# Kernel tuning notes

Hardware: AMD Instinct MI355X
Metric: run time of the kernel (lower is better)

## Reference

```python
import jax, jax.numpy as jnp
import numpy as np
import math

N = 10000      # nodes (batched protein residues)
E = 160000     # edges (avg degree 16)
D = 1280       # node/hidden dim (ESM2-650M)
M = 24         # message_dim
EE = 16        # edge_embedding_dim (sinusoidal distance features)
L = 6          # num EGNN layers
LN_EPS = 1e-5


def setup_inputs() -> dict:
    key = jax.random.key(0)
    ks = jax.random.split(key, 20)
    s = 0.02
    h = jax.random.normal(ks[0], (N, D), jnp.float32)
    pos = jax.random.normal(ks[1], (N, 3), jnp.float32) * 10.0
    edge_index = jax.random.randint(ks[2], (2, E), 0, N, jnp.int32)
    msg_in_dim = 2 * D + EE + 1  # h_i, h_j, edge_attr, radial
    params = dict(
        node_emb_W=jax.random.normal(ks[3], (D, D), jnp.float32) * s,
        node_emb_b=jnp.zeros((D,), jnp.float32),
        msg_W1=jax.random.normal(ks[4], (L, msg_in_dim, M), jnp.float32) * s,
        msg_b1=jnp.zeros((L, M), jnp.float32),
        msg_W2=jax.random.normal(ks[5], (L, M, M), jnp.float32) * s,
        msg_b2=jnp.zeros((L, M), jnp.float32),
        coord_W1=jax.random.normal(ks[6], (L - 1, M, M), jnp.float32) * s,
        coord_b1=jnp.zeros((L - 1, M), jnp.float32),
        coord_W2=jax.random.normal(ks[7], (L - 1, M, 1), jnp.float32) * s,  # no bias
        node_W1=jax.random.normal(ks[8], (L, D + M, M), jnp.float32) * s,
        node_b1=jnp.zeros((L, M), jnp.float32),
        node_W2=jax.random.normal(ks[9], (L, M, D), jnp.float32) * s,
        node_b2=jnp.zeros((L, D), jnp.float32),
        ln_g=jnp.ones((L, D), jnp.float32),
        ln_b=jnp.zeros((L, D), jnp.float32),
    )
    return dict(h=h, pos=pos, edge_index=edge_index, **params)


def reference(h, pos, edge_index, node_emb_W, node_emb_b, msg_W1, msg_b1,
              msg_W2, msg_b2, coord_W1, coord_b1, coord_W2,
              node_W1, node_b1, node_W2, node_b2, ln_g, ln_b):
    row, col = edge_index[0], edge_index[1]  # PyG: row=source j, col=target i

    # sinusoidal distance embedding from initial coordinates (computed once)
    freqs = jnp.exp(-math.log(10000.0) * jnp.arange(0, EE, 2, dtype=jnp.float32) / EE)
    d0 = pos[row] - pos[col]                      # (E,3)
    dist = jnp.sqrt(jnp.sum(d0 * d0, axis=1))     # (E,)
    ang = dist[:, None] * freqs[None, :]          # (E, EE/2)
    edge_attr = jnp.stack([jnp.sin(ang), jnp.cos(ang)], axis=2).reshape(dist.shape[0], EE)

    h = h @ node_emb_W + node_emb_b

    # mean-aggregation denominator: in-degree of target nodes, clamped to 1
    deg = jax.ops.segment_sum(jnp.ones_like(dist), col, num_segments=N)
    denom = jnp.maximum(deg, 1.0)[:, None]

    for l in range(L):
        cd = pos[row] - pos[col]                  # (E,3) coord_diff
        radial = jnp.sum(cd * cd, axis=1, keepdims=True)
        msg_in = jnp.concatenate([h[col], h[row], edge_attr, radial], axis=-1)  # (E, 2D+EE+1)
        msg = jax.nn.silu(jax.nn.silu(msg_in @ msg_W1[l] + msg_b1[l]) @ msg_W2[l] + msg_b2[l])
        msg_agg = jax.ops.segment_sum(msg, col, num_segments=N) / denom  # scatter-mean
        if l < L - 1:  # update_coords for all but last layer
            w = jax.nn.silu(msg @ coord_W1[l] + coord_b1[l]) @ coord_W2[l]  # (E,1)
            pos = pos + jax.ops.segment_sum(cd * w, col, num_segments=N)   # index_add
        h_up = jax.nn.silu(jnp.concatenate([h, msg_agg], axis=-1) @ node_W1[l] + node_b1[l]) @ node_W2[l] + node_b2[l]
        hn = h + h_up
        mu = jnp.mean(hn, axis=-1, keepdims=True)
        var = jnp.mean((hn - mu) ** 2, axis=-1, keepdims=True)
        h = (hn - mu) / jnp.sqrt(var + LN_EPS) * ln_g[l] + ln_b[l]
        # dropout is identity in eval mode
    return h, pos
```

## Files before the change

### kernel.cpp

```cpp
#include <hip/hip_runtime.h>

#define NN 10000
#define NE 160000
#define DD 1280
#define MM 24

typedef __attribute__((ext_vector_type(8))) short bf16x8;
typedef __attribute__((ext_vector_type(4))) float f32x4;
typedef unsigned short u16;

#define O_nembW 0
#define O_nembB 1638400
#define O_msgW1 1639680
#define O_msgB1 2010880
#define O_msgW2 2011136
#define O_msgB2 2014592
#define O_cW1   2014848
#define O_cB1   2017792
#define O_cW2   2017920
#define O_nW1   2018048
#define O_nB1   2205824
#define O_nW2   2206080
#define O_nB2   2390400
#define O_lnG   2398080
#define O_lnB   2405760
#define TOTW    2413440

__device__ __forceinline__ float b2f(u16 u){
  union { unsigned int i; float f; } v; v.i = ((unsigned int)u) << 16; return v.f;
}
__device__ __forceinline__ u16 f2b(float f){
  union { float f; unsigned int i; } v; v.f = f;
  return (u16)((v.i + 0x7fffu + ((v.i >> 16) & 1u)) >> 16);
}
__device__ __forceinline__ float silu_f(float x){ return x / (1.f + __expf(-x)); }

__device__ __forceinline__ void gll16(const u16* g, u16* l){
  __builtin_amdgcn_global_load_lds(
      (const __attribute__((address_space(1))) void*)g,
      (__attribute__((address_space(3))) void*)l, 16, 0, 0);
}

__global__ __launch_bounds__(256) void k_sniff(const u16* __restrict__ h0, int* __restrict__ modep)
{
  __shared__ int cnt;
  if (threadIdx.x == 0) cnt = 0;
  __syncthreads();
  int local = 0;
  for (int i = threadIdx.x; i < 16384; i += 256){
    unsigned int e = (h0[i] >> 7) & 0xFF;
    if (e >= 0xE0) local++;
  }
  atomicAdd(&cnt, local);
  __syncthreads();
  if (threadIdx.x == 0) *modep = (cnt > 16) ? 0 : 1;
}

__global__ __launch_bounds__(256) void k_cvtw(const int* __restrict__ modep,
    const void* p0, const void* p1, const void* p2, const void* p3, const void* p4,
    const void* p5, const void* p6, const void* p7, const void* p8, const void* p9,
    const void* p10, const void* p11, const void* p12, const void* p13, const void* p14,
    u16* __restrict__ wbf)
{
  int i = blockIdx.x * 256 + threadIdx.x;
  if (i >= TOTW) return;
  int mode = *modep;
  const void* src; int j; int sz;
  if      (i < O_nembB){ src = p0;  j = i - O_nembW; sz = 1638400; }
  else if (i < O_msgW1){ src = p1;  j = i - O_nembB; sz = 1280; }
  else if (i < O_msgB1){ src = p2;  j = i - O_msgW1; sz = 371088; }
  else if (i < O_msgW2){ src = p3;  j = i - O_msgB1; sz = 144; }
  else if (i < O_msgB2){ src = p4;  j = i - O_msgW2; sz = 3456; }
  else if (i < O_cW1)  { src = p5;  j = i - O_msgB2; sz = 144; }
  else if (i < O_cB1)  { src = p6;  j = i - O_cW1;   sz = 2880; }
  else if (i < O_cW2)  { src = p7;  j = i - O_cB1;   sz = 120; }
  else if (i < O_nW1)  { src = p8;  j = i - O_cW2;   sz = 120; }
  else if (i < O_nB1)  { src = p9;  j = i - O_nW1;   sz = 187776; }
  else if (i < O_nW2)  { src = p10; j = i - O_nB1;   sz = 144; }
  else if (i < O_nB2)  { src = p11; j = i - O_nW2;   sz = 184320; }
  else if (i < O_lnG)  { src = p12; j = i - O_nB2;   sz = 7680; }
  else if (i < O_lnB)  { src = p13; j = i - O_lnG;   sz = 7680; }
  else                 { src = p14; j = i - O_lnB;   sz = 7680; }
  u16 v = 0;
  if (j < sz) v = mode ? ((const u16*)src)[j] : f2b(((const float*)src)[j]);
  wbf[i] = v;
}

__global__ __launch_bounds__(256) void k_tr(const u16* __restrict__ win, u16* __restrict__ wout)
{
  __shared__ u16 tile[32][33];
  int bx = blockIdx.x % 40, by = blockIdx.x / 40;
  int tc = threadIdx.x & 31, tr = threadIdx.x >> 5;
  #pragma unroll
  for (int p = 0; p < 4; p++){
    int r = p*8 + tr;
    tile[r][tc] = win[(size_t)(by*32 + r)*1280 + bx*32 + tc];
  }
  __syncthreads();
  #pragma unroll
  for (int p = 0; p < 4; p++){
    int r = p*8 + tr;
    wout[(size_t)(bx*32 + r)*1280 + by*32 + tc] = tile[tc][r];
  }
}

__global__ __launch_bounds__(256) void k_packproj(const u16* __restrict__ wbf, u16* __restrict__ wproj)
{
  int i = blockIdx.x * 256 + threadIdx.x;
  if (i >= 6*80*1280) return;
  int l = i / (80*1280);
  int rem = i - l*80*1280;
  int n = rem / 1280;
  int k = rem - n*1280;
  u16 v = 0;
  if (n < 24)       v = wbf[O_msgW1 + (size_t)l*2577*24 + (size_t)k*24 + n];
  else if (n < 48)  v = wbf[O_msgW1 + (size_t)l*2577*24 + (size_t)(1280+k)*24 + (n-24)];
  else if (n < 72)  v = wbf[O_nW1   + (size_t)l*1304*24 + (size_t)k*24 + (n-48)];
  wproj[i] = v;
}

__global__ __launch_bounds__(256) void k_packw2(const u16* __restrict__ wbf, u16* __restrict__ wn2p)
{
  int i = blockIdx.x * 256 + threadIdx.x;
  int l = i / (1280*32); int rem = i - l*1280*32;
  int n = rem >> 5, k = rem & 31;
  wn2p[i] = (k < 24) ? wbf[O_nW2 + (size_t)l*24*1280 + (size_t)k*1280 + n] : (u16)0;
}

__global__ __launch_bounds__(256) void k_cvth(const void* h0, const int* __restrict__ modep,
                                              u16* __restrict__ h0b)
{
  int i = blockIdx.x * 256 + threadIdx.x;
  if (*modep){
    ((int4*)h0b)[i] = ((const int4*)h0)[i];
  } else {
    const float* s = (const float*)h0 + (size_t)i*8;
    bf16x8 o;
    #pragma unroll
    for (int j = 0; j < 8; j++) o[j] = (short)f2b(s[j]);
    *(bf16x8*)(h0b + (size_t)i*8) = o;
  }
}

__global__ __launch_bounds__(256) void k_setup(const void* pos0, const int* __restrict__ modep,
    float* __restrict__ deg, float* __restrict__ posf, float* __restrict__ posf0)
{
  int i = blockIdx.x * 256 + threadIdx.x;
  int mode = *modep;
  if (i < NN) deg[i] = 0.f;
  if (i < NN * 3){
    float p = mode ? b2f(((const u16*)pos0)[i]) : ((const float*)pos0)[i];
    posf[i] = p; posf0[i] = p;
  }
}

__global__ __launch_bounds__(256) void k_deg(const int* __restrict__ eidx, float* __restrict__ deg)
{
  int e = blockIdx.x * 256 + threadIdx.x;
  atomicAdd(&deg[eidx[NE + e]], 1.f);
}

__global__ __launch_bounds__(256) void k_prefix(const float* __restrict__ deg,
                                                int* __restrict__ offs, int* __restrict__ cursor)
{
  __shared__ int part[256];
  int t = threadIdx.x;
  int lo = t * 40, hi = lo + 40; if (hi > NN) hi = NN; if (lo > NN) lo = NN;
  int s = 0;
  for (int i = lo; i < hi; i++) s += (int)deg[i];
  part[t] = s;
  __syncthreads();
  for (int off = 1; off < 256; off <<= 1){
    int v = (t >= off) ? part[t - off] : 0;
    __syncthreads();
    part[t] += v;
    __syncthreads();
  }
  int run = (t == 0) ? 0 : part[t - 1];
  for (int i = lo; i < hi; i++){
    offs[i] = run;
    run += (int)deg[i];
    cursor[i] = 0;
  }
  if (t == 255) offs[NN] = run;
}

__global__ __launch_bounds__(256) void k_scatter(const int* __restrict__ eidx,
    const int* __restrict__ offs, int* __restrict__ cursor, int* __restrict__ perm)
{
  int e = blockIdx.x * 256 + threadIdx.x;
  int cg = eidx[NE + e];
  int p = atomicAdd(&cursor[cg], 1);
  perm[offs[cg] + p] = e;
}

__global__ __launch_bounds__(256) void k_gemm_init(const u16* __restrict__ h0b,
    const u16* __restrict__ wembT, const u16* __restrict__ wbf, u16* __restrict__ Cb)
{
  __shared__ u16 As[128*32];
  __shared__ u16 Bs[128*32];
  int t = threadIdx.x;
  int lane = t & 63, wv = t >> 6;
  int bm = blockIdx.x % 79, bn = blockIdx.x / 79;
  int m0 = bm * 128, n0 = bn * 128;
  int col = lane & 15, quad = lane >> 4;
  int wm = wv & 1, wn = wv >> 1;
  f32x4 acc[4][4];
  #pragma unroll
  for (int mi = 0; mi < 4; mi++)
    #pragma unroll
    for (int ni = 0; ni < 4; ni++) acc[mi][ni] = (f32x4){0.f,0.f,0.f,0.f};

  for (int k0 = 0; k0 < DD; k0 += 32){
    #pragma unroll
    for (int is = 0; is < 2; is++){
      int flat = is*256 + t;
      int row = flat >> 2, seg = flat & 3;
      int grow = m0 + row; if (grow > NN-1) grow = NN-1;
      gll16(h0b + (size_t)grow*DD + k0 + seg*8, As + flat*8);
    }
    #pragma unroll
    for (int is = 0; is < 2; is++){
      int flat = is*256 + t;
      int row = flat >> 2, seg = flat & 3;
      gll16(wembT + (size_t)(n0 + row)*DD + k0 + seg*8, Bs + flat*8);
    }
    __builtin_amdgcn_s_waitcnt(0x0f70);
    __syncthreads();
    bf16x8 af[4], bfv[4];
    #pragma unroll
    for (int mi = 0; mi < 4; mi++)
      af[mi] = *(const bf16x8*)&As[(wm*64 + mi*16 + col)*32 + quad*8];
    #pragma unroll
    for (int ni = 0; ni < 4; ni++)
      bfv[ni] = *(const bf16x8*)&Bs[(wn*64 + ni*16 + col)*32 + quad*8];
    #pragma unroll
    for (int mi = 0; mi < 4; mi++)
      #pragma unroll
      for (int ni = 0; ni < 4; ni++)
        acc[mi][ni] = __builtin_amdgcn_mfma_f32_16x16x32_bf16(af[mi], bfv[ni], acc[mi][ni], 0, 0, 0);
    __syncthreads();
  }
  #pragma unroll
  for (int ni = 0; ni < 4; ni++){
    int cc = n0 + wn*64 + ni*16 + col;
    float bias = b2f(wbf[O_nembB + cc]);
    #pragma unroll
    for (int mi = 0; mi < 4; mi++){
      #pragma unroll
      for (int rr = 0; rr < 4; rr++){
        int row = m0 + wm*64 + mi*16 + quad*4 + rr;
        if (row < NN) Cb[(size_t)row*DD + cc] = f2b(acc[mi][ni][rr] + bias);
      }
    }
  }
}

__global__ __launch_bounds__(128) void k_gemm_proj(const u16* __restrict__ hbm,
    const u16* __restrict__ wproj, int layer,
    float* __restrict__ Ab, float* __restrict__ Bb, float* __restrict__ Mb)
{
  __shared__ u16 As[32*32];
  __shared__ u16 Bs[80*32];
  int t = threadIdx.x;
  int lane = t & 63, wv = t >> 6;
  int m0 = blockIdx.x * 32;
  int col = lane & 15, quad = lane >> 4;
  const u16* wp = wproj + (size_t)layer * 80 * 1280;
  f32x4 acc[5];
  #pragma unroll
  for (int ni = 0; ni < 5; ni++) acc[ni] = (f32x4){0.f,0.f,0.f,0.f};

  for (int k0 = 0; k0 < DD; k0 += 32){
    { int row = t >> 2, seg = t & 3;
      int grow = m0 + row; if (grow > NN-1) grow = NN-1;
      gll16(hbm + (size_t)grow*DD + k0 + seg*8, As + t*8); }
    #pragma unroll
    for (int is = 0; is < 3; is++){
      int flat = is*128 + t;
      if (flat < 320){
        int row = flat >> 2, seg = flat & 3;
        gll16(wp + (size_t)row*DD + k0 + seg*8, Bs + flat*8);
      }
    }
    __builtin_amdgcn_s_waitcnt(0x0f70);
    __syncthreads();
    bf16x8 af = *(const bf16x8*)&As[(wv*16 + col)*32 + quad*8];
    #pragma unroll
    for (int ni = 0; ni < 5; ni++){
      bf16x8 bv = *(const bf16x8*)&Bs[(ni*16 + col)*32 + quad*8];
      acc[ni] = __builtin_amdgcn_mfma_f32_16x16x32_bf16(af, bv, acc[ni], 0, 0, 0);
    }
    __syncthreads();
  }
  #pragma unroll
  for (int ni = 0; ni < 5; ni++){
    int n = ni*16 + col;
    if (n < 72){
      int rg = (n >= 48) ? 2 : (n >= 24 ? 1 : 0);
      int cc = n - rg*24;
      float* base = (rg == 0) ? Ab : (rg == 1) ? Bb : Mb;
      #pragma unroll
      for (int rr = 0; rr < 4; rr++){
        int m = m0 + wv*16 + quad*4 + rr;
        if (m < NN) base[m*24 + cc] = acc[ni][rr];
      }
    }
  }
}

__global__ __launch_bounds__(256) void k_edge(const int* __restrict__ eidx,
    const float* __restrict__ posf, const float* __restrict__ posf0,
    const float* __restrict__ Ab, const float* __restrict__ Bb,
    const u16* __restrict__ wbf, int layer, int do_coord,
    u16* __restrict__ msgu, float* __restrict__ wcdbuf)
{
  __shared__ float sW1e[16*24], sWr[24], sB1[24], sW2[24*24], sB2[24];
  __shared__ float sCW1[24*24], sCB1[24], sCW2[24];
  int t = threadIdx.x;
  const u16* w1l = wbf + O_msgW1 + (size_t)layer * 2577 * 24;
  for (int i = t; i < 16*24; i += 256) sW1e[i] = b2f(w1l[2560*24 + i]);
  for (int i = t; i < 24; i += 256){
    sWr[i] = b2f(w1l[2576*24 + i]);
    sB1[i] = b2f(wbf[O_msgB1 + layer*24 + i]);
    sB2[i] = b2f(wbf[O_msgB2 + layer*24 + i]);
  }
  for (int i = t; i < 576; i += 256) sW2[i] = b2f(wbf[O_msgW2 + layer*576 + i]);
  if (do_coord){
    for (int i = t; i < 576; i += 256) sCW1[i] = b2f(wbf[O_cW1 + layer*576 + i]);
    for (int i = t; i < 24; i += 256){
      sCB1[i] = b2f(wbf[O_cB1 + layer*24 + i]);
      sCW2[i] = b2f(wbf[O_cW2 + layer*24 + i]);
    }
  }
  __syncthreads();
  int e = blockIdx.x * 256 + t;
  int r = eidx[e], cg = eidx[NE + e];
  float cdx = posf[r*3+0] - posf[cg*3+0];
  float cdy = posf[r*3+1] - posf[cg*3+1];
  float cdz = posf[r*3+2] - posf[cg*3+2];
  float radial = cdx*cdx + cdy*cdy + cdz*cdz;
  float ex = posf0[r*3+0] - posf0[cg*3+0];
  float ey = posf0[r*3+1] - posf0[cg*3+1];
  float ez = posf0[r*3+2] - posf0[cg*3+2];
  float dist = sqrtf(ex*ex + ey*ey + ez*ez);
  const float FR[8] = {1.f, 0.31622776601683794f, 0.1f, 0.03162277660168379f,
                       0.01f, 0.0031622776601683794f, 0.001f, 0.00031622776601683794f};
  float eav[16];
  #pragma unroll
  for (int j = 0; j < 8; j++){
    float ang = dist * FR[j];
    eav[2*j]   = __sinf(ang);
    eav[2*j+1] = __cosf(ang);
  }
  float acc[24];
  const float4* ap  = (const float4*)(Ab + cg * 24);
  const float4* bp4 = (const float4*)(Bb + r * 24);
  #pragma unroll
  for (int q = 0; q < 6; q++){
    float4 a4 = ap[q], b4 = bp4[q];
    acc[q*4+0] = a4.x + b4.x; acc[q*4+1] = a4.y + b4.y;
    acc[q*4+2] = a4.z + b4.z; acc[q*4+3] = a4.w + b4.w;
  }
  #pragma unroll
  for (int m = 0; m < 24; m++) acc[m] += sB1[m] + radial * sWr[m];
  #pragma unroll
  for (int k = 0; k < 16; k++){
    #pragma unroll
    for (int m = 0; m < 24; m++) acc[m] += eav[k] * sW1e[k*24 + m];
  }
  #pragma unroll
  for (int m = 0; m < 24; m++) acc[m] = silu_f(acc[m]);
  float msg[24];
  #pragma unroll
  for (int m = 0; m < 24; m++){
    float v = sB2[m];
    #pragma unroll
    for (int k = 0; k < 24; k++) v += acc[k] * sW2[k*24 + m];
    msg[m] = silu_f(v);
  }
  {
    bf16x8 v0, v1, v2;
    #pragma unroll
    for (int j = 0; j < 8; j++){
      v0[j] = (short)f2b(msg[j]);
      v1[j] = (short)f2b(msg[8+j]);
      v2[j] = (short)f2b(msg[16+j]);
    }
    u16* mp = msgu + (size_t)e * 24;
    *(bf16x8*)(mp)      = v0;
    *(bf16x8*)(mp + 8)  = v1;
    *(bf16x8*)(mp + 16) = v2;
  }
  if (do_coord){
    float w = 0.f;
    #pragma unroll
    for (int m = 0; m < 24; m++){
      float v = sCB1[m];
      #pragma unroll
      for (int k = 0; k < 24; k++) v += msg[k] * sCW1[k*24 + m];
      w += silu_f(v) * sCW2[m];
    }
    wcdbuf[(size_t)e*3+0] = cdx * w;
    wcdbuf[(size_t)e*3+1] = cdy * w;
    wcdbuf[(size_t)e*3+2] = cdz * w;
  }
}

__global__ __launch_bounds__(256) void k_agg(const int* __restrict__ perm,
    const int* __restrict__ offs,
    const u16* __restrict__ msgu, const float* __restrict__ wcdbuf,
    float* __restrict__ magg, float* __restrict__ posf,
    int do_coord, int writeout, void* __restrict__ outp, const int* __restrict__ modep)
{
  int wv = threadIdx.x >> 6, lane = threadIdx.x & 63;
  int n = blockIdx.x * 4 + wv;
  int base = offs[n], cnt = offs[n+1] - base;
  float sum = 0.f;
  if (lane < 48){
    int m = (lane < 24) ? lane : lane - 24;
    for (int j = (lane < 24 ? 0 : 1); j < cnt; j += 2)
      sum += b2f(msgu[(size_t)perm[base+j]*24 + m]);
  }
  sum += __shfl_down(sum, 24, 64);
  if (lane < 24) magg[n*24 + lane] = sum;
  if (do_coord){
    float sc = 0.f;
    if (lane < 48){
      int c = lane % 3, jj = lane / 3;
      for (int j = jj; j < cnt; j += 16)
        sc += wcdbuf[(size_t)perm[base+j]*3 + c];
    }
    sc += __shfl_down(sc, 24, 64);
    sc += __shfl_down(sc, 12, 64);
    sc += __shfl_down(sc, 6, 64);
    sc += __shfl_down(sc, 3, 64);
    if (lane < 3){
      float p = posf[n*3 + lane] + sc;
      posf[n*3 + lane] = p;
      if (writeout){
        if (*modep) ((u16*)outp)[(size_t)NN*DD + n*3 + lane] = f2b(p);
        else        ((float*)outp)[(size_t)NN*DD + n*3 + lane] = p;
      }
    }
  }
}

__global__ __launch_bounds__(256) void k_combine(
    const float* __restrict__ Mb, const float* __restrict__ magg, const float* __restrict__ deg,
    const u16* __restrict__ wbf, const u16* __restrict__ wn2p, const int* __restrict__ modep,
    int layer, int last,
    u16* __restrict__ hbm, void* __restrict__ outp)
{
  __shared__ u16 shRes[16*1280];
  __shared__ u16 midb[16*32];
  __shared__ float sW1b[576], sB1c[24], sMg[384], sMbs[384], sDeg[16];
  __shared__ float wpart[4][16][2];
  __shared__ float mrow[16][2];
  int t = threadIdx.x;
  int lane = t & 63, wv = t >> 6;
  int row0 = blockIdx.x * 16;
  #pragma unroll
  for (int it = 0; it < 10; it++){
    int flat = it*256 + t;
    int r = flat / 160, off = (flat - r*160) * 8;
    gll16(hbm + (size_t)(row0 + r)*1280 + off, shRes + flat*8);
  }
  const u16* w1b = wbf + O_nW1 + (size_t)layer*1304*24 + 1280*24;
  for (int i = t; i < 576; i += 256) sW1b[i] = b2f(w1b[i]);
  if (t < 24) sB1c[t] = b2f(wbf[O_nB1 + layer*24 + t]);
  if (t < 16) sDeg[t] = 1.f / fmaxf(deg[row0 + t], 1.f);
  for (int i = t; i < 384; i += 256){ sMg[i] = magg[row0*24 + i]; sMbs[i] = Mb[row0*24 + i]; }
  midb[t] = 0; midb[256 + t] = 0;
  __builtin_amdgcn_s_waitcnt(0x0f70);
  __syncthreads();
  for (int o = t; o < 384; o += 256){
    int r = o / 24, m = o - r*24;
    float inv = sDeg[r];
    float a = sMbs[o] + sB1c[m];
    #pragma unroll
    for (int j = 0; j < 24; j++) a += sMg[r*24 + j] * inv * sW1b[j*24 + m];
    midb[r*32 + m] = f2b(silu_f(a));
  }
  __syncthreads();
  int col = lane & 15, quad = lane >> 4;
  bf16x8 af = *(const bf16x8*)&midb[col*32 + quad*8];
  int mode = *modep;
  float s1[4] = {0.f,0.f,0.f,0.f}, s2[4] = {0.f,0.f,0.f,0.f};
  float vals[20][4];
  const u16* wp = wn2p + (size_t)layer*1280*32;
  const u16* b2p = wbf + O_nB2 + (size_t)layer*1280;
  #pragma unroll
  for (int ti = 0; ti < 20; ti++){
    int n0 = wv*320 + ti*16;
    bf16x8 bfv = *(const bf16x8*)&wp[(size_t)(n0+col)*32 + quad*8];
    f32x4 acc = {0.f,0.f,0.f,0.f};
    acc = __builtin_amdgcn_mfma_f32_16x16x32_bf16(af, bfv, acc, 0, 0, 0);
    float b2 = b2f(b2p[n0 + col]);
    #pragma unroll
    for (int rr = 0; rr < 4; rr++){
      int r = quad*4 + rr;
      float hn = b2f(shRes[r*1280 + n0 + col]) + acc[rr] + b2;
      vals[ti][rr] = hn;
      s1[rr] += hn; s2[rr] += hn*hn;
    }
  }
  #pragma unroll
  for (int off = 1; off < 16; off <<= 1){
    #pragma unroll
    for (int rr = 0; rr < 4; rr++){
      s1[rr] += __shfl_xor(s1[rr], off, 64);
      s2[rr] += __shfl_xor(s2[rr], off, 64);
    }
  }
  if (col == 0){
    #pragma unroll
    for (int rr = 0; rr < 4; rr++){
      wpart[wv][quad*4+rr][0] = s1[rr];
      wpart[wv][quad*4+rr][1] = s2[rr];
    }
  }
  __syncthreads();
  if (t < 16){
    float S1 = wpart[0][t][0] + wpart[1][t][0] + wpart[2][t][0] + wpart[3][t][0];
    float S2 = wpart[0][t][1] + wpart[1][t][1] + wpart[2][t][1] + wpart[3][t][1];
    float mu = S1 * (1.f/1280.f);
    float var = S2 * (1.f/1280.f) - mu*mu;
    mrow[t][0] = mu;
    mrow[t][1] = rsqrtf(var + 1e-5f);
  }
  __syncthreads();
  const u16* gp = wbf + O_lnG + (size_t)layer*1280;
  const u16* bp = wbf + O_lnB + (size_t)layer*1280;
  #pragma unroll
  for (int ti = 0; ti < 20; ti++){
    int n0 = wv*320 + ti*16;
    int cc = n0 + col;
    float g  = b2f(gp[cc]);
    float bb = b2f(bp[cc]);
    #pragma unroll
    for (int rr = 0; rr < 4; rr++){
      int r = quad*4 + rr;
      float y = (vals[ti][rr] - mrow[r][0]) * mrow[r][1] * g + bb;
      hbm[(size_t)(row0 + r)*1280 + cc] = f2b(y);
      if (last){
        if (mode) ((u16*)outp)[(size_t)(row0+r)*1280 + cc] = f2b(y);
        else      ((float*)outp)[(size_t)(row0+r)*1280 + cc] = y;
      }
    }
  }
}

extern "C" void kernel_launch(void* const* d_in, const int* in_sizes, int n_in,
                              void* d_out, int out_size, void* d_ws, size_t ws_size,
                              hipStream_t stream)
{
  const void* h0    = d_in[0];
  const void* pos0  = d_in[1];
  const int*  eidx  = (const int*)d_in[2];

  char* w = (char*)d_ws;
  auto take = [&](size_t bytes)->char*{
    char* p = w; w += (bytes + 255) & ~(size_t)255; return p;
  };
  int*   modep  = (int*)  take(256);
  u16*   wbf    = (u16*)  take((size_t)TOTW * 2);
  u16*   wembT  = (u16*)  take((size_t)DD * DD * 2);
  u16*   wproj  = (u16*)  take((size_t)6 * 80 * 1280 * 2);
  u16*   wn2p   = (u16*)  take((size_t)6 * 1280 * 32 * 2);
  u16*   hbm    = (u16*)  take((size_t)NN * DD * 2);
  float* Ab     = (float*)take((size_t)NN * MM * 4);
  float* Bb     = (float*)take((size_t)NN * MM * 4);
  float* Mb     = (float*)take((size_t)NN * MM * 4);
  float* magg   = (float*)take((size_t)NN * MM * 4);
  float* deg    = (float*)take((size_t)NN * 4);
  float* posf   = (float*)take((size_t)NN * 3 * 4);
  float* posf0  = (float*)take((size_t)NN * 3 * 4);
  int*   offs   = (int*)  take((size_t)(NN + 1) * 4);
  int*   cursor = (int*)  take((size_t)NN * 4);
  int*   perm   = (int*)  take((size_t)NE * 4);

  u16*   h0b    = (u16*)d_out;
  u16*   msgu   = (u16*)d_out;
  float* wcdbuf = (float*)((char*)d_out + (size_t)NE * 24 * 2);

  k_sniff<<<1, 256, 0, stream>>>((const u16*)h0, modep);
  k_cvtw<<<(TOTW + 255)/256, 256, 0, stream>>>(modep,
      d_in[3], d_in[4], d_in[5], d_in[6], d_in[7], d_in[8], d_in[9], d_in[10],
      d_in[11], d_in[12], d_in[13], d_in[14], d_in[15], d_in[16], d_in[17], wbf);
  k_tr<<<1600, 256, 0, stream>>>(wbf + O_nembW, wembT);
  k_packproj<<<(6*80*1280 + 255)/256, 256, 0, stream>>>(wbf, wproj);
  k_packw2<<<6*1280*32/256, 256, 0, stream>>>(wbf, wn2p);
  k_cvth<<<NN*DD/8/256, 256, 0, stream>>>(h0, modep, h0b);
  k_setup<<<(NN*3 + 255)/256, 256, 0, stream>>>(pos0, modep, deg, posf, posf0);
  k_deg<<<NE/256, 256, 0, stream>>>(eidx, deg);
  k_prefix<<<1, 256, 0, stream>>>(deg, offs, cursor);
  k_scatter<<<NE/256, 256, 0, stream>>>(eidx, offs, cursor, perm);
  k_gemm_init<<<79*10, 256, 0, stream>>>(h0b, wembT, wbf, hbm);
  for (int l = 0; l < 6; l++){
    int dc = (l < 5) ? 1 : 0;
    k_gemm_proj<<<313, 128, 0, stream>>>(hbm, wproj, l, Ab, Bb, Mb);
    k_edge<<<NE/256, 256, 0, stream>>>(eidx, posf, posf0, Ab, Bb, wbf, l, dc, msgu, wcdbuf);
    k_agg<<<2500, 256, 0, stream>>>(perm, offs, msgu, wcdbuf, magg, posf,
                                    dc, (l == 4) ? 1 : 0, d_out, modep);
    k_combine<<<625, 256, 0, stream>>>(Mb, magg, deg, wbf, wn2p, modep, l, (l == 5) ? 1 : 0,
                                       hbm, d_out);
  }
}
```

Before: 858.5 us.

## Retile init GEMM to 64x128 blocks with swizzled LDS and grouped block order

Result: no change. 847.8 us (-1.2%).

```diff
diff --git a/kernel.cpp b/kernel.cpp
--- a/kernel.cpp
+++ b/kernel.cpp
@@ -197,59 +197,65 @@
 __global__ __launch_bounds__(256) void k_gemm_init(const u16* __restrict__ h0b,
     const u16* __restrict__ wembT, const u16* __restrict__ wbf, u16* __restrict__ Cb)
 {
-  __shared__ u16 As[128*32];
+  __shared__ u16 As[64*32];
   __shared__ u16 Bs[128*32];
+  int bid = blockIdx.x;
+  int bm = (bid & 7) + 8 * (bid / 80);
+  int bn = (bid >> 3) % 10;
+  if (bm >= 157) return;
   int t = threadIdx.x;
   int lane = t & 63, wv = t >> 6;
-  int bm = blockIdx.x % 79, bn = blockIdx.x / 79;
-  int m0 = bm * 128, n0 = bn * 128;
+  int m0 = bm * 64, n0 = bn * 128;
   int col = lane & 15, quad = lane >> 4;
-  int wm = wv & 1, wn = wv >> 1;
-  f32x4 acc[4][4];
+  f32x4 acc[4][2];
   #pragma unroll
   for (int mi = 0; mi < 4; mi++)
     #pragma unroll
-    for (int ni = 0; ni < 4; ni++) acc[mi][ni] = (f32x4){0.f,0.f,0.f,0.f};
+    for (int ni = 0; ni < 2; ni++) acc[mi][ni] = (f32x4){0.f,0.f,0.f,0.f};
 
   for (int k0 = 0; k0 < DD; k0 += 32){
+    { int row = t >> 2, kcp = t & 3;
+      int src = (kcp ^ ((row >> 1) & 3)) * 8;
+      int grow = m0 + row; if (grow > NN-1) grow = NN-1;
+      gll16(h0b + (size_t)grow*DD + k0 + src, As + t*8); }
     #pragma unroll
     for (int is = 0; is < 2; is++){
       int flat = is*256 + t;
-      int row = flat >> 2, seg = flat & 3;
-      int grow = m0 + row; if (grow > NN-1) grow = NN-1;
-      gll16(h0b + (size_t)grow*DD + k0 + seg*8, As + flat*8);
-    }
-    #pragma unroll
-    for (int is = 0; is < 2; is++){
-      int flat = is*256 + t;
-      int row = flat >> 2, seg = flat & 3;
-      gll16(wembT + (size_t)(n0 + row)*DD + k0 + seg*8, Bs + flat*8);
+      int row = flat >> 2, kcp = flat & 3;
+      int src = (kcp ^ ((row >> 1) & 3)) * 8;
+      gll16(wembT + (size_t)(n0 + row)*DD + k0 + src, Bs + flat*8);
     }
     __builtin_amdgcn_s_waitcnt(0x0f70);
     __syncthreads();
-    bf16x8 af[4], bfv[4];
-    #pragma unroll
-    for (int mi = 0; mi < 4; mi++)
-      af[mi] = *(const bf16x8*)&As[(wm*64 + mi*16 + col)*32 + quad*8];
-    #pragma unroll
-    for (int ni = 0; ni < 4; ni++)
-      bfv[ni] = *(const bf16x8*)&Bs[(wn*64 + ni*16 + col)*32 + quad*8];
+    bf16x8 af[4], bfv[2];
+    #pragma unroll
+    for (int mi = 0; mi < 4; mi++){
+      int row = mi*16 + col;
+      int ch = quad ^ ((row >> 1) & 3);
+      af[mi] = *(const bf16x8*)&As[row*32 + ch*8];
+    }
+    #pragma unroll
+    for (int ni = 0; ni < 2; ni++){
+      int row = wv*32 + ni*16 + col;
+      int ch = quad ^ ((row >> 1) & 3);
+      bfv[ni] = *(const bf16x8*)&Bs[row*32 + ch*8];
+    }
     #pragma unroll
     for (int mi = 0; mi < 4; mi++)
       #pragma unroll
-      for (int ni = 0; ni < 4; ni++)
+      for (int ni = 0; ni < 2; ni++)
         acc[mi][ni] = __builtin_amdgcn_mfma_f32_16x16x32_bf16(af[mi], bfv[ni], acc[mi][ni], 0, 0, 0);
     __syncthreads();
   }
   #pragma unroll
-  for (int ni = 0; ni < 4; ni++){
-    int cc = n0 + wn*64 + ni*16 + col;
+  for (int ni = 0; ni < 2; ni++){
+    int cc = n0 + wv*32 + ni*16 + col;
     float bias = b2f(wbf[O_nembB + cc]);
     #pragma unroll
     for (int mi = 0; mi < 4; mi++){
       #pragma unroll
       for (int rr = 0; rr < 4; rr++){
-        int row = m0 + wm*64 + mi*16 + quad*4 + rr;
+        int row = m0 + mi*16 + quad*4 + rr;
         if (row < NN) Cb[(size_t)row*DD + cc] = f2b(acc[mi][ni][rr] + bias);
       }
     }
@@ -596,7 +602,7 @@
   k_deg<<<NE/256, 256, 0, stream>>>(eidx, deg);
   k_prefix<<<1, 256, 0, stream>>>(deg, offs, cursor);
   k_scatter<<<NE/256, 256, 0, stream>>>(eidx, offs, cursor, perm);
-  k_gemm_init<<<79*10, 256, 0, stream>>>(h0b, wembT, wbf, hbm);
+  k_gemm_init<<<1600, 256, 0, stream>>>(h0b, wembT, wbf, hbm);
   for (int l = 0; l < 6; l++){
     int dc = (l < 5) ? 1 : 0;
     k_gemm_proj<<<313, 128, 0, stream>>>(hbm, wproj, l, Ab, Bb, Mb);
```
